# Optimization experiments

Hardware: AMD Instinct MI355X
Metric: run time of the kernel (lower is better)

## Reference

```python
import jax, jax.numpy as jnp
import numpy as np

B, S, F_IN, D, H, L, E, DFF, OUT = 16, 512, 46, 256, 8, 6, 8, 1024, 3


def _ln(x, s, b, eps=1e-5):
    m = x.mean(-1, keepdims=True)
    v = ((x - m) ** 2).mean(-1, keepdims=True)
    return (x - m) / jnp.sqrt(v + eps) * s + b


def _mha(q_in, kv_in, qkv_w, qkv_b, out_w, out_b, h):
    # torch nn.MultiheadAttention (batch_first), eval mode (no dropout)
    d = q_in.shape[-1]
    dh = d // h
    wq, wk, wv = jnp.split(qkv_w, 3, axis=0)
    bq, bk, bv = jnp.split(qkv_b, 3)
    q = (q_in @ wq.T + bq).reshape(q_in.shape[0], q_in.shape[1], h, dh)
    k = (kv_in @ wk.T + bk).reshape(kv_in.shape[0], kv_in.shape[1], h, dh)
    v = (kv_in @ wv.T + bv).reshape(kv_in.shape[0], kv_in.shape[1], h, dh)
    attn = jax.nn.softmax(jnp.einsum('bqhd,bkhd->bhqk', q, k) / jnp.sqrt(jnp.float32(dh)), axis=-1)
    o = jnp.einsum('bhqk,bkhd->bqhd', attn, v).reshape(q_in.shape[0], q_in.shape[1], d)
    return o @ out_w.T + out_b


def _moe(x, gate_w, gate_b, e_w1, e_b1, e_w2, e_b2, top_k=2):
    # Faithful to source: EVERY expert runs its dense FFN over all tokens,
    # then outputs are mixed by the top-k gate weights (zero for unrouted experts).
    logits = x @ gate_w.T + gate_b                      # (B,S,E)
    tk_logits, tk_idx = jax.lax.top_k(logits, top_k)    # (B,S,K)
    tk_probs = jax.nn.softmax(tk_logits, axis=-1)
    onehot = jax.nn.one_hot(tk_idx, logits.shape[-1], dtype=x.dtype)  # (B,S,K,E)
    weights = (onehot * tk_probs[..., None]).sum(-2)    # (B,S,E)
    hid = jax.nn.gelu(jnp.einsum('bsd,efd->bsef', x, e_w1) + e_b1, approximate=False)  # (B,S,E,DFF)
    out_e = jnp.einsum('bsef,edf->bsed', hid, e_w2) + e_b2                             # (B,S,E,D)
    out = jnp.einsum('bsed,bse->bsd', out_e, weights)
    probs = jax.nn.softmax(logits, axis=-1)
    aux = logits.shape[-1] * jnp.sum(probs.mean(axis=(0, 1)) ** 2)
    return out, aux


def _posenc(s, d):
    pos = jnp.arange(s, dtype=jnp.float32)[:, None]
    div = jnp.exp(jnp.arange(0, d, 2, dtype=jnp.float32) * (-np.log(10000.0) / d))
    pe = jnp.zeros((s, d), jnp.float32)
    pe = pe.at[:, 0::2].set(jnp.sin(pos * div)).at[:, 1::2].set(jnp.cos(pos * div))
    return pe


def _forward(x, in_w, in_b, l_qkv_w, l_qkv_b, l_out_w, l_out_b, gate_w, gate_b,
             e_w1, e_b1, e_w2, e_b2, ln1_s, ln1_b, ln2_s, ln2_b,
             p_qkv_w, p_qkv_b, p_out_w, p_out_b,
             a_w1, a_b1, a_ln1s, a_ln1b, a_w2, a_b2, a_ln2s, a_ln2b, a_w3, a_b3,
             pr_w1, pr_b1, pr_ln1s, pr_ln1b, pr_w2, pr_b2, pr_ln2s, pr_ln2b, pr_w3, pr_b3):
    h = x @ in_w.T + in_b + _posenc(x.shape[1], D)[None]
    aux_total = jnp.float32(0.0)
    # NB: source builds ModuleList([encoder_layer]*L) with the SAME instance -> shared weights
    for _ in range(L):
        attn = _mha(h, h, l_qkv_w, l_qkv_b, l_out_w, l_out_b, H)
        h = _ln(h + attn, ln1_s, ln1_b)
        moe_out, aux = _moe(h, gate_w, gate_b, e_w1, e_b1, e_w2, e_b2)
        aux_total = aux_total + aux
        h = _ln(h + moe_out, ln2_s, ln2_b)
    pooled = _mha(h[:, -1:, :], h, p_qkv_w, p_qkv_b, p_out_w, p_out_b, H)[:, 0]  # (B,D)
    # action head: Linear -> GELU -> LN -> Linear -> GELU -> LN -> Linear
    a = jax.nn.gelu(pooled @ a_w1.T + a_b1, approximate=False)
    a = _ln(a, a_ln1s, a_ln1b)
    a = jax.nn.gelu(a @ a_w2.T + a_b2, approximate=False)
    a = _ln(a, a_ln2s, a_ln2b)
    action = a @ a_w3.T + a_b3
    # profit head: Linear -> LN -> GELU -> Linear -> LN -> GELU -> Linear
    p = jax.nn.gelu(_ln(pooled @ pr_w1.T + pr_b1, pr_ln1s, pr_ln1b), approximate=False)
    p = jax.nn.gelu(_ln(p @ pr_w2.T + pr_b2, pr_ln2s, pr_ln2b), approximate=False)
    profit = p @ pr_w3.T + pr_b3
    return action, profit, aux_total


def setup_inputs() -> dict:
    key = jax.random.key(0)
    ks = iter(jax.random.split(key, 64))
    def w(shape, scale=0.02):
        return jax.random.normal(next(ks), shape, jnp.float32) * scale
    d2, d4 = D // 2, D // 4
    return dict(
        x=jax.random.normal(next(ks), (B, S, F_IN), jnp.float32),
        in_w=w((D, F_IN)), in_b=jnp.zeros(D),
        l_qkv_w=w((3 * D, D)), l_qkv_b=jnp.zeros(3 * D), l_out_w=w((D, D)), l_out_b=jnp.zeros(D),
        gate_w=w((E, D)), gate_b=jnp.zeros(E),
        e_w1=w((E, DFF, D)), e_b1=jnp.zeros((E, DFF)), e_w2=w((E, D, DFF)), e_b2=jnp.zeros((E, D)),
        ln1_s=jnp.ones(D), ln1_b=jnp.zeros(D), ln2_s=jnp.ones(D), ln2_b=jnp.zeros(D),
        p_qkv_w=w((3 * D, D)), p_qkv_b=jnp.zeros(3 * D), p_out_w=w((D, D)), p_out_b=jnp.zeros(D),
        a_w1=w((d2, D)), a_b1=jnp.zeros(d2), a_ln1s=jnp.ones(d2), a_ln1b=jnp.zeros(d2),
        a_w2=w((d4, d2)), a_b2=jnp.zeros(d4), a_ln2s=jnp.ones(d4), a_ln2b=jnp.zeros(d4),
        a_w3=w((OUT, d4)), a_b3=jnp.zeros(OUT),
        pr_w1=w((D, D)), pr_b1=jnp.zeros(D), pr_ln1s=jnp.ones(D), pr_ln1b=jnp.zeros(D),
        pr_w2=w((d2, D)), pr_b2=jnp.zeros(d2), pr_ln2s=jnp.ones(d2), pr_ln2b=jnp.zeros(d2),
        pr_w3=w((1, d2)), pr_b3=jnp.zeros(1),
    )


def reference(x, in_w, in_b, l_qkv_w, l_qkv_b, l_out_w, l_out_b, gate_w, gate_b,
              e_w1, e_b1, e_w2, e_b2, ln1_s, ln1_b, ln2_s, ln2_b,
              p_qkv_w, p_qkv_b, p_out_w, p_out_b,
              a_w1, a_b1, a_ln1s, a_ln1b, a_w2, a_b2, a_ln2s, a_ln2b, a_w3, a_b3,
              pr_w1, pr_b1, pr_ln1s, pr_ln1b, pr_w2, pr_b2, pr_ln2s, pr_ln2b, pr_w3, pr_b3):
    return _forward(x, in_w, in_b, l_qkv_w, l_qkv_b, l_out_w, l_out_b, gate_w, gate_b,
                    e_w1, e_b1, e_w2, e_b2, ln1_s, ln1_b, ln2_s, ln2_b,
                    p_qkv_w, p_qkv_b, p_out_w, p_out_b,
                    a_w1, a_b1, a_ln1s, a_ln1b, a_w2, a_b2, a_ln2s, a_ln2b, a_w3, a_b3,
                    pr_w1, pr_b1, pr_ln1s, pr_ln1b, pr_w2, pr_b2, pr_ln2s, pr_ln2b, pr_w3, pr_b3)
```

## Files before the change

### kernel.cpp

```cpp
#include <hip/hip_runtime.h>
#include <hip/hip_bf16.h>
#include <math.h>


typedef __bf16 bf16;
typedef __bf16 bf16x8 __attribute__((ext_vector_type(8)));
typedef __bf16 bf16x4 __attribute__((ext_vector_type(4)));
typedef float f32x4 __attribute__((ext_vector_type(4)));

#define NIN 41

#define GLOAD_LDS(g, l)                                                    \
    __builtin_amdgcn_global_load_lds(                                      \
        (const __attribute__((address_space(1))) void*)(g),                \
        (__attribute__((address_space(3))) void*)(l), 16, 0, 0)

struct InTab {
    const void* src[NIN];
    unsigned off[NIN];
    unsigned n[NIN];
};

__device__ __forceinline__ float gelu_exact(float x) {
    return 0.5f * x * (1.0f + erff(x * 0.70710678118654752f));
}

__global__ void sniff_kernel(const unsigned* __restrict__ xw, int* __restrict__ flag) {
    __shared__ int cnt;
    if (threadIdx.x == 0) cnt = 0;
    __syncthreads();
    const unsigned w = xw[threadIdx.x];
    const unsigned ex = (w >> 7) & 0xFFu;
    if (ex >= 107u && ex <= 133u) atomicAdd(&cnt, 1);
    __syncthreads();
    if (threadIdx.x == 0) *flag = (cnt >= 192) ? 1 : 0;
}

__global__ __launch_bounds__(256) void convert_kernel(
    InTab tab, bf16* __restrict__ dst_base, const int* __restrict__ flag) {
    const unsigned g0 = blockIdx.x * 1024u;
    int inp = 0;
#pragma unroll
    for (int i = 1; i < NIN; i++)
        if (g0 >= tab.off[i]) inp = i;
    const unsigned n = tab.n[inp];
    const unsigned i0 = g0 - tab.off[inp] + threadIdx.x * 4u;
    if (i0 >= n) return;
    const int isbf = *flag;
    bf16* dst = dst_base + tab.off[inp];
    const unsigned end = (i0 + 4u > n) ? n : i0 + 4u;
    if (isbf) {
        const unsigned short* s = (const unsigned short*)tab.src[inp];
        for (unsigned i = i0; i < end; i++) ((unsigned short*)dst)[i] = s[i];
    } else {
        const float* s = (const float*)tab.src[inp];
        for (unsigned i = i0; i < end; i++) dst[i] = (bf16)s[i];
    }
}

__global__ void out_convert_kernel(const float* __restrict__ st,
                                   const float* __restrict__ auxsums,
                                   void* __restrict__ out,
                                   const int* __restrict__ flag) {
    const int i = threadIdx.x;
    if (i >= 65) return;
    float v;
    if (i == 64) {
        float tot = 0.0f;
        for (int l = 0; l < 6; l++)
            for (int e = 0; e < 8; e++) {
                const float mn = auxsums[l * 8 + e] * (1.0f / 8192.0f);
                tot += 8.0f * mn * mn;
            }
        v = tot;
    } else {
        v = st[i];
    }
    if (*flag) ((bf16*)out)[i] = (bf16)v;
    else       ((float*)out)[i] = v;
}

#define SWZ(r, c) (((r) * 8 + ((c) ^ ((r) & 7))) * 8)

template <int BM, int BN, int WM, int WN, bool VTOUT>
__global__ __launch_bounds__(256) void gemm_bt(
    const bf16* __restrict__ A, const bf16* __restrict__ W,
    const bf16* __restrict__ bias, bf16* __restrict__ C,
    int M, int N, int K, bf16* __restrict__ vT) {
    constexpr int BK = 64;
    __shared__ alignas(16) bf16 As[BM * BK];
    __shared__ alignas(16) bf16 Ws[BN * BK];
    const int bm0 = blockIdx.x * BM, bn0 = blockIdx.y * BN;
    const int tid = threadIdx.x;
    const int wave = tid >> 6, lane = tid & 63;
    constexpr int WCOLS = BN / WN;
    const int wm0 = (wave / WCOLS) * WM, wn0 = (wave % WCOLS) * WN;
    constexpr int MT = WM / 16, NT = WN / 16;
    f32x4 acc[MT][NT] = {};
    const int frow = lane & 15, fquad = lane >> 4;

    constexpr int AIT = BM / 32, BIT = BN / 32;
    const bf16* ag[AIT];
    const bf16* bg[BIT];
    unsigned al[AIT], bl[BIT];
#pragma unroll
    for (int i = 0; i < AIT; i++) {
        const int d = wave * (BM * 2) + i * 64 + lane;
        const int r = d >> 3, c = ((d & 7) ^ (r & 7)) * 8;
        ag[i] = A + (size_t)(bm0 + r) * K + c;
        al[i] = (unsigned)(wave * (BM * 2) + i * 64) * 8u;
    }
#pragma unroll
    for (int i = 0; i < BIT; i++) {
        const int d = wave * (BN * 2) + i * 64 + lane;
        const int r = d >> 3, c = ((d & 7) ^ (r & 7)) * 8;
        bg[i] = W + (size_t)(bn0 + r) * K + c;
        bl[i] = (unsigned)(wave * (BN * 2) + i * 64) * 8u;
    }

    for (int k0 = 0; k0 < K; k0 += BK) {
#pragma unroll
        for (int i = 0; i < AIT; i++) GLOAD_LDS(ag[i] + k0, &As[al[i]]);
#pragma unroll
        for (int i = 0; i < BIT; i++) GLOAD_LDS(bg[i] + k0, &Ws[bl[i]]);
        __syncthreads();
#pragma unroll
        for (int ks = 0; ks < BK / 32; ks++) {
            bf16x8 af[MT], bfr[NT];
#pragma unroll
            for (int mt = 0; mt < MT; mt++) {
                const int r = wm0 + mt * 16 + frow;
                af[mt] = *(const bf16x8*)&As[SWZ(r, ks * 4 + fquad)];
            }
#pragma unroll
            for (int nt = 0; nt < NT; nt++) {
                const int r = wn0 + nt * 16 + frow;
                bfr[nt] = *(const bf16x8*)&Ws[SWZ(r, ks * 4 + fquad)];
            }
#pragma unroll
            for (int mt = 0; mt < MT; mt++)
#pragma unroll
                for (int nt = 0; nt < NT; nt++)
                    acc[mt][nt] = __builtin_amdgcn_mfma_f32_16x16x32_bf16(
                        af[mt], bfr[nt], acc[mt][nt], 0, 0, 0);
        }
        __syncthreads();
    }

#pragma unroll
    for (int mt = 0; mt < MT; mt++)
#pragma unroll
        for (int nt = 0; nt < NT; nt++) {
            const int gn = bn0 + wn0 + nt * 16 + frow;
            const float bv = (float)bias[gn];
#pragma unroll
            for (int r = 0; r < 4; r++) {
                const int gm = bm0 + wm0 + mt * 16 + fquad * 4 + r;
                const float v = acc[mt][nt][r] + bv;
                if (VTOUT && gn >= 512) {
                    const int d = gn - 512;
                    const int bb = gm >> 9, s = gm & 511;
                    vT[((size_t)(bb * 8 + (d >> 5)) * 32 + (d & 31)) * 512 + s] = (bf16)v;
                } else {
                    C[(size_t)gm * N + gn] = (bf16)v;
                }
            }
        }
}

__global__ __launch_bounds__(256) void gemm_moe_w1(
    const bf16* __restrict__ A, const bf16* __restrict__ Wb,
    const bf16* __restrict__ biasb, bf16* __restrict__ hid0,
    bf16* __restrict__ hid1, const int* __restrict__ list,
    const int* __restrict__ tile_ex, const int* __restrict__ ntiles) {
    constexpr int BM = 128, BN = 128, BK = 64, WM = 64, WN = 64;
    constexpr int N = 1024, K = 256;
    const int slot = (blockIdx.x >= 71) ? 1 : 0;
    const int xi = blockIdx.x - slot * 71;
    if (xi >= ntiles[slot]) return;
    __shared__ alignas(16) bf16 As[BM * BK];
    __shared__ alignas(16) bf16 Ws[BN * BK];
    const int* mylist = list + slot * 9216;
    const int e = tile_ex[slot * 72 + xi];
    const bf16* W = Wb + (size_t)e * N * K;
    const bf16* bias = biasb + e * N;
    bf16* C = slot ? hid1 : hid0;
    const int bm0 = xi * BM, bn0 = blockIdx.y * BN;
    const int tid = threadIdx.x;
    const int wave = tid >> 6, lane = tid & 63;
    constexpr int WCOLS = BN / WN;
    const int wm0 = (wave / WCOLS) * WM, wn0 = (wave % WCOLS) * WN;
    constexpr int MT = WM / 16, NT = WN / 16;
    f32x4 acc[MT][NT] = {};
    const int frow = lane & 15, fquad = lane >> 4;

    const bf16* ag[4];
    const bf16* bg[4];
    unsigned al[4], bl[4];
#pragma unroll
    for (int i = 0; i < 4; i++) {
        const int d = wave * 256 + i * 64 + lane;
        const int r = d >> 3, c = ((d & 7) ^ (r & 7)) * 8;
        ag[i] = A + (size_t)mylist[bm0 + r] * K + c;
        al[i] = (unsigned)(wave * 256 + i * 64) * 8u;
        bg[i] = W + (size_t)(bn0 + r) * K + c;
        bl[i] = al[i];
    }

    for (int k0 = 0; k0 < K; k0 += BK) {
#pragma unroll
        for (int i = 0; i < 4; i++) GLOAD_LDS(ag[i] + k0, &As[al[i]]);
#pragma unroll
        for (int i = 0; i < 4; i++) GLOAD_LDS(bg[i] + k0, &Ws[bl[i]]);
        __syncthreads();
#pragma unroll
        for (int ks = 0; ks < 2; ks++) {
            bf16x8 af[MT], bfr[NT];
#pragma unroll
            for (int mt = 0; mt < MT; mt++) {
                const int r = wm0 + mt * 16 + frow;
                af[mt] = *(const bf16x8*)&As[SWZ(r, ks * 4 + fquad)];
            }
#pragma unroll
            for (int nt = 0; nt < NT; nt++) {
                const int r = wn0 + nt * 16 + frow;
                bfr[nt] = *(const bf16x8*)&Ws[SWZ(r, ks * 4 + fquad)];
            }
#pragma unroll
            for (int mt = 0; mt < MT; mt++)
#pragma unroll
                for (int nt = 0; nt < NT; nt++)
                    acc[mt][nt] = __builtin_amdgcn_mfma_f32_16x16x32_bf16(
                        af[mt], bfr[nt], acc[mt][nt], 0, 0, 0);
        }
        __syncthreads();
    }

#pragma unroll
    for (int mt = 0; mt < MT; mt++)
#pragma unroll
        for (int nt = 0; nt < NT; nt++) {
            const int gn = bn0 + wn0 + nt * 16 + frow;
            const float bv = (float)bias[gn];
#pragma unroll
            for (int r = 0; r < 4; r++) {
                const int gm = bm0 + wm0 + mt * 16 + fquad * 4 + r;
                C[(size_t)gm * N + gn] = (bf16)gelu_exact(acc[mt][nt][r] + bv);
            }
        }
}

__global__ __launch_bounds__(256) void gemm_moe_w2(
    const bf16* __restrict__ hid0, const bf16* __restrict__ hid1,
    const bf16* __restrict__ Wb, const bf16* __restrict__ biasb,
    bf16* __restrict__ moe0, bf16* __restrict__ moe1,
    const int* __restrict__ list, const float* __restrict__ lw,
    const int* __restrict__ tile_ex, const int* __restrict__ ntiles) {
    constexpr int BM = 128, BN = 64, BK = 64, WM = 32;
    constexpr int N = 256, K = 1024;
    const int slot = (blockIdx.x >= 71) ? 1 : 0;
    const int xi = blockIdx.x - slot * 71;
    if (xi >= ntiles[slot]) return;
    __shared__ alignas(16) bf16 As[BM * BK];
    __shared__ alignas(16) bf16 Ws[BN * BK];
    const bf16* A = slot ? hid1 : hid0;
    bf16* C = slot ? moe1 : moe0;
    const int* mylist = list + slot * 9216;
    const float* mylw = lw + slot * 9216;
    const int e = tile_ex[slot * 72 + xi];
    const bf16* W = Wb + (size_t)e * N * K;
    const bf16* bias = biasb + e * N;
    const int bm0 = xi * BM, bn0 = blockIdx.y * BN;
    const int tid = threadIdx.x;
    const int wave = tid >> 6, lane = tid & 63;
    const int wm0 = wave * WM;
    constexpr int MT = WM / 16, NT = 4;
    f32x4 acc[MT][NT] = {};
    const int frow = lane & 15, fquad = lane >> 4;

    const bf16* ag[4];
    const bf16* bg[2];
    unsigned al[4], bl[2];
#pragma unroll
    for (int i = 0; i < 4; i++) {
        const int d = wave * 256 + i * 64 + lane;
        const int r = d >> 3, c = ((d & 7) ^ (r & 7)) * 8;
        ag[i] = A + (size_t)(bm0 + r) * K + c;
        al[i] = (unsigned)(wave * 256 + i * 64) * 8u;
    }
#pragma unroll
    for (int i = 0; i < 2; i++) {
        const int d = wave * 128 + i * 64 + lane;
        const int r = d >> 3, c = ((d & 7) ^ (r & 7)) * 8;
        bg[i] = W + (size_t)(bn0 + r) * K + c;
        bl[i] = (unsigned)(wave * 128 + i * 64) * 8u;
    }

    for (int k0 = 0; k0 < K; k0 += BK) {
#pragma unroll
        for (int i = 0; i < 4; i++) GLOAD_LDS(ag[i] + k0, &As[al[i]]);
#pragma unroll
        for (int i = 0; i < 2; i++) GLOAD_LDS(bg[i] + k0, &Ws[bl[i]]);
        __syncthreads();
#pragma unroll
        for (int ks = 0; ks < 2; ks++) {
            bf16x8 af[MT], bfr[NT];
#pragma unroll
            for (int mt = 0; mt < MT; mt++) {
                const int r = wm0 + mt * 16 + frow;
                af[mt] = *(const bf16x8*)&As[SWZ(r, ks * 4 + fquad)];
            }
#pragma unroll
            for (int nt = 0; nt < NT; nt++) {
                const int r = nt * 16 + frow;
                bfr[nt] = *(const bf16x8*)&Ws[SWZ(r, ks * 4 + fquad)];
            }
#pragma unroll
            for (int mt = 0; mt < MT; mt++)
#pragma unroll
                for (int nt = 0; nt < NT; nt++)
                    acc[mt][nt] = __builtin_amdgcn_mfma_f32_16x16x32_bf16(
                        af[mt], bfr[nt], acc[mt][nt], 0, 0, 0);
        }
        __syncthreads();
    }

#pragma unroll
    for (int mt = 0; mt < MT; mt++)
#pragma unroll
        for (int nt = 0; nt < NT; nt++) {
            const int gn = bn0 + nt * 16 + frow;
            const float bv = (float)bias[gn];
#pragma unroll
            for (int r = 0; r < 4; r++) {
                const int gm = bm0 + wm0 + mt * 16 + fquad * 4 + r;
                const float v = acc[mt][nt][r] + bv;
                C[(size_t)mylist[gm] * 256 + gn] = (bf16)(mylw[gm] * v);
            }
        }
}

__global__ __launch_bounds__(256) void input_proj_kernel(
    const bf16* __restrict__ x, const bf16* __restrict__ w,
    const bf16* __restrict__ b, bf16* __restrict__ h) {
    const int m = blockIdx.x, t = threadIdx.x;
    __shared__ float xs[46];
    if (t < 46) xs[t] = (float)x[m * 46 + t];
    __syncthreads();
    float acc = (float)b[t];
#pragma unroll
    for (int k = 0; k < 46; k++) acc += xs[k] * (float)w[t * 46 + k];
    const int s = m & 511;
    const int i = t >> 1;
    const float dv = expf((float)(2 * i) * (-9.210340371976184f / 256.0f));
    const float ang = (float)s * dv;
    const float pe = (t & 1) ? cosf(ang) : sinf(ang);
    h[(size_t)m * 256 + t] = (bf16)(acc + pe);
}

__global__ __launch_bounds__(256) void ln_kernel(
    bf16* __restrict__ h, const bf16* __restrict__ a0,
    const bf16* __restrict__ a1, const bf16* __restrict__ s,
    const bf16* __restrict__ b) {
    const int wv = threadIdx.x >> 6, lane = threadIdx.x & 63;
    const int m = blockIdx.x * 8 + wv * 2 + (lane >> 5);
    const int c0 = (lane & 31) * 8;
    const size_t off = (size_t)m * 256 + c0;
    bf16x8 hv = *(const bf16x8*)&h[off];
    bf16x8 av = *(const bf16x8*)&a0[off];
    bf16x8 bv2 = *(const bf16x8*)&a1[off];
    float x[8];
    float s1 = 0.0f, s2 = 0.0f;
#pragma unroll
    for (int j = 0; j < 8; j++) {
        x[j] = (float)hv[j] + (float)av[j] + (float)bv2[j];
        s1 += x[j];
        s2 += x[j] * x[j];
    }
#pragma unroll
    for (int msk = 1; msk < 32; msk <<= 1) {
        s1 += __shfl_xor(s1, msk, 64);
        s2 += __shfl_xor(s2, msk, 64);
    }
    const float mean = s1 * (1.0f / 256.0f);
    const float var = fmaxf(s2 * (1.0f / 256.0f) - mean * mean, 0.0f);
    const float inv = rsqrtf(var + 1e-5f);
    bf16x8 sv = *(const bf16x8*)&s[c0];
    bf16x8 bv = *(const bf16x8*)&b[c0];
    bf16x8 o;
#pragma unroll
    for (int j = 0; j < 8; j++)
        o[j] = (bf16)((x[j] - mean) * inv * (float)sv[j] + (float)bv[j]);
    *(bf16x8*)&h[off] = o;
}

__global__ __launch_bounds__(256) void proj_gate_ln_kernel(
    const bf16* __restrict__ A, const bf16* __restrict__ W,
    const bf16* __restrict__ bias, bf16* __restrict__ h,
    const bf16* __restrict__ lns, const bf16* __restrict__ lnb,
    const bf16* __restrict__ gw, const bf16* __restrict__ gb,
    int* __restrict__ top_e, float* __restrict__ top_w,
    int* __restrict__ g_hist, float* __restrict__ aux_sums) {
    __shared__ alignas(16) bf16 As[32 * 64];
    __shared__ alignas(16) bf16 Ws[256 * 64];
    __shared__ alignas(16) bf16 hs[32 * 264];
    __shared__ alignas(16) bf16 gws[8 * 264];
    __shared__ float rws1[4][32], rws2[4][32];
    __shared__ float meanv[32], invv[32];
    __shared__ float lg[256];
    __shared__ int sh_hist[16];
    __shared__ float sh_aux[8];

    const int bm0 = blockIdx.x * 32;
    const int tid = threadIdx.x;
    const int wave = tid >> 6, lane = tid & 63;
    const int wn0 = (wave & 3) * 64;
    const int frow = lane & 15, fquad = lane >> 4;
    f32x4 acc[2][4] = {};

    const int da = wave * 64 + lane;
    const int ra = da >> 3, ca = ((da & 7) ^ (ra & 7)) * 8;
    const bf16* ag = A + (size_t)(bm0 + ra) * 256 + ca;
    const unsigned al = (unsigned)(wave * 64) * 8u;
    const bf16* bg[8];
    unsigned bl[8];
#pragma unroll
    for (int i = 0; i < 8; i++) {
        const int d = wave * 512 + i * 64 + lane;
        const int r = d >> 3, c = ((d & 7) ^ (r & 7)) * 8;
        bg[i] = W + (size_t)r * 256 + c;
        bl[i] = (unsigned)(wave * 512 + i * 64) * 8u;
    }

    {
        const int rr = tid >> 3, ccb = (tid & 7) * 32;
        const bf16* src = &h[(size_t)(bm0 + rr) * 256 + ccb];
        bf16x8 v0 = *(const bf16x8*)&src[0];
        bf16x8 v1 = *(const bf16x8*)&src[8];
        bf16x8 v2 = *(const bf16x8*)&src[16];
        bf16x8 v3 = *(const bf16x8*)&src[24];
        bf16* dst = &hs[rr * 264 + ccb];
        *(bf16x8*)&dst[0] = v0;
        *(bf16x8*)&dst[8] = v1;
        *(bf16x8*)&dst[16] = v2;
        *(bf16x8*)&dst[24] = v3;
    }
    {
        const int e = tid >> 5, k = (tid & 31) * 8;
        *(bf16x8*)&gws[e * 264 + k] = *(const bf16x8*)&gw[e * 256 + k];
    }
    if (tid < 16) sh_hist[tid] = 0;
    if (tid < 8) sh_aux[tid] = 0.0f;

    for (int k0 = 0; k0 < 256; k0 += 64) {
        GLOAD_LDS(ag + k0, &As[al]);
#pragma unroll
        for (int i = 0; i < 8; i++) GLOAD_LDS(bg[i] + k0, &Ws[bl[i]]);
        __syncthreads();
#pragma unroll
        for (int ks = 0; ks < 2; ks++) {
            bf16x8 af[2], bfr[4];
#pragma unroll
            for (int mt = 0; mt < 2; mt++)
                af[mt] = *(const bf16x8*)&As[SWZ(mt * 16 + frow, ks * 4 + fquad)];
#pragma unroll
            for (int nt = 0; nt < 4; nt++)
                bfr[nt] = *(const bf16x8*)&Ws[SWZ(wn0 + nt * 16 + frow, ks * 4 + fquad)];
#pragma unroll
            for (int mt = 0; mt < 2; mt++)
#pragma unroll
                for (int nt = 0; nt < 4; nt++)
                    acc[mt][nt] = __builtin_amdgcn_mfma_f32_16x16x32_bf16(
                        af[mt], bfr[nt], acc[mt][nt], 0, 0, 0);
        }
        __syncthreads();
    }

    float s1v[2][4] = {}, s2v[2][4] = {};
#pragma unroll
    for (int mt = 0; mt < 2; mt++)
#pragma unroll
        for (int nt = 0; nt < 4; nt++) {
            const int gn = wn0 + nt * 16 + frow;
            const float bv = (float)bias[gn];
#pragma unroll
            for (int r = 0; r < 4; r++) {
                const int row = mt * 16 + fquad * 4 + r;
                const float x = acc[mt][nt][r] + bv + (float)hs[row * 264 + gn];
                acc[mt][nt][r] = x;
                s1v[mt][r] += x;
                s2v[mt][r] += x * x;
            }
        }
#pragma unroll
    for (int mt = 0; mt < 2; mt++)
#pragma unroll
        for (int r = 0; r < 4; r++) {
#pragma unroll
            for (int m = 1; m < 16; m <<= 1) {
                s1v[mt][r] += __shfl_xor(s1v[mt][r], m, 64);
                s2v[mt][r] += __shfl_xor(s2v[mt][r], m, 64);
            }
        }
    if (frow == 0) {
#pragma unroll
        for (int mt = 0; mt < 2; mt++)
#pragma unroll
            for (int r = 0; r < 4; r++) {
                const int row = mt * 16 + fquad * 4 + r;
                rws1[wave][row] = s1v[mt][r];
                rws2[wave][row] = s2v[mt][r];
            }
    }
    __syncthreads();
    if (tid < 32) {
        const float a = rws1[0][tid] + rws1[1][tid] + rws1[2][tid] + rws1[3][tid];
        const float c2 = rws2[0][tid] + rws2[1][tid] + rws2[2][tid] + rws2[3][tid];
        const float mean = a * (1.0f / 256.0f);
        const float var = fmaxf(c2 * (1.0f / 256.0f) - mean * mean, 0.0f);
        meanv[tid] = mean;
        invv[tid] = rsqrtf(var + 1e-5f);
    }
    __syncthreads();

#pragma unroll
    for (int mt = 0; mt < 2; mt++)
#pragma unroll
        for (int nt = 0; nt < 4; nt++) {
            const int gn = wn0 + nt * 16 + frow;
            const float sg = (float)lns[gn], bgn = (float)lnb[gn];
#pragma unroll
            for (int r = 0; r < 4; r++) {
                const int row = mt * 16 + fquad * 4 + r;
                const float o = (acc[mt][nt][r] - meanv[row]) * invv[row] * sg + bgn;
                hs[row * 264 + gn] = (bf16)o;
            }
        }
    __syncthreads();

    {
        const int rr = tid >> 3, ccb = (tid & 7) * 32;
        bf16* dst = &h[(size_t)(bm0 + rr) * 256 + ccb];
        const bf16* src = &hs[rr * 264 + ccb];
        *(bf16x8*)&dst[0] = *(const bf16x8*)&src[0];
        *(bf16x8*)&dst[8] = *(const bf16x8*)&src[8];
        *(bf16x8*)&dst[16] = *(const bf16x8*)&src[16];
        *(bf16x8*)&dst[24] = *(const bf16x8*)&src[24];
    }
    {
        const int row = tid >> 3, e = tid & 7;
        float acg = (float)gb[e];
        for (int k = 0; k < 256; k += 8) {
            bf16x8 hv = *(const bf16x8*)&hs[row * 264 + k];
            bf16x8 wv = *(const bf16x8*)&gws[e * 264 + k];
#pragma unroll
            for (int q = 0; q < 8; q++) acg += (float)hv[q] * (float)wv[q];
        }
        lg[row * 8 + e] = acg;
    }
    __syncthreads();

    if (tid < 32) {
        const int tok = bm0 + tid;
        float l[8];
#pragma unroll
        for (int j = 0; j < 8; j++) l[j] = lg[tid * 8 + j];
        int i0 = 0;
#pragma unroll
        for (int j = 1; j < 8; j++)
            if (l[j] > l[i0]) i0 = j;
        int i1 = -1;
#pragma unroll
        for (int j = 0; j < 8; j++)
            if (j != i0 && (i1 < 0 || l[j] > l[i1])) i1 = j;
        const float p0 = 1.0f / (1.0f + expf(l[i1] - l[i0]));
        top_e[tok] = i0;         top_w[tok] = p0;
        top_e[8192 + tok] = i1;  top_w[8192 + tok] = 1.0f - p0;
        atomicAdd(&sh_hist[i0], 1);
        atomicAdd(&sh_hist[8 + i1], 1);
        const float mx = l[i0];
        float se = 0.0f;
#pragma unroll
        for (int j = 0; j < 8; j++) { l[j] = expf(l[j] - mx); se += l[j]; }
        const float si = 1.0f / se;
#pragma unroll
        for (int j = 0; j < 8; j++) atomicAdd(&sh_aux[j], l[j] * si);
    }
    __syncthreads();
    if (tid < 16) g_hist[blockIdx.x * 16 + tid] = sh_hist[tid];
    if (tid < 8) atomicAdd(&aux_sums[tid], sh_aux[tid]);
}

__global__ __launch_bounds__(256) void scatter_route_kernel(
    const int* __restrict__ g_hist, const int* __restrict__ top_e,
    const float* __restrict__ top_w, int* __restrict__ ntiles,
    int* __restrict__ tile_ex, int* __restrict__ list, float* __restrict__ lw) {
    __shared__ int gh[256][16];
    __shared__ int ps[16][8];
    __shared__ int s_cnt[16], s_pre[16], s_off[16], pos[16];
    const int tid = threadIdx.x;
    for (int i = tid; i < 4096; i += 256) gh[i >> 4][i & 15] = g_hist[i];
    __syncthreads();
    if (tid < 128) {
        const int se = tid >> 3, ch = tid & 7;
        int s = 0;
        for (int b = ch * 32; b < ch * 32 + 32; b++) s += gh[b][se];
        ps[se][ch] = s;
    }
    __syncthreads();
    if (tid < 16) {
        int run = 0;
        for (int ch = 0; ch < 8; ch++) run += ps[tid][ch];
        const int b0 = (int)blockIdx.x * 4;
        int pre = 0;
        for (int ch = 0; ch < (b0 >> 5); ch++) pre += ps[tid][ch];
        for (int b = b0 & ~31; b < b0; b++) pre += gh[b][tid];
        s_cnt[tid] = run;
        s_pre[tid] = pre;
    }
    __syncthreads();
    if (tid < 2) {
        const int slot = tid;
        int o = 0;
        for (int e2 = 0; e2 < 8; e2++) {
            s_off[slot * 8 + e2] = o;
            const int nt = (s_cnt[slot * 8 + e2] + 127) >> 7;
            if (blockIdx.x == 0)
                for (int t = 0; t < nt; t++) tile_ex[slot * 72 + (o >> 7) + t] = e2;
            o += nt << 7;
        }
        if (blockIdx.x == 0) ntiles[slot] = o >> 7;
    }
    __syncthreads();
    if (tid < 16) pos[tid] = s_off[tid] + s_pre[tid];
    __syncthreads();
    if (blockIdx.x == 0) {
        for (int idx = tid; idx < 16 * 128; idx += 256) {
            const int seg = idx >> 7, i = idx & 127;
            const int slot = seg >> 3;
            const int start = s_off[seg] + s_cnt[seg];
            const int end = s_off[seg] + ((s_cnt[seg] + 127) & ~127);
            const int p = start + i;
            if (p < end) {
                list[slot * 9216 + p] = 8192;
                lw[slot * 9216 + p] = 0.0f;
            }
        }
    }
    if (tid < 128) {
        const int tok = blockIdx.x * 128 + tid;
#pragma unroll
        for (int slot = 0; slot < 2; slot++) {
            const int e = top_e[slot * 8192 + tok];
            const float w = top_w[slot * 8192 + tok];
            const int idx = atomicAdd(&pos[slot * 8 + e], 1);
            list[slot * 9216 + idx] = tok;
            lw[slot * 9216 + idx] = w;
        }
    }
}

__global__ __launch_bounds__(256) void attn_kernel(
    const bf16* __restrict__ qkv, const bf16* __restrict__ vT,
    bf16* __restrict__ aout) {
    __shared__ alignas(16) bf16 P[32][520];
    __shared__ float wsum[4][32];
    __shared__ float sinv[32];
    const int s0 = blockIdx.x * 32;
    const int b = blockIdx.y >> 3, hh = blockIdx.y & 7;
    const int tid = threadIdx.x, wave = tid >> 6, lane = tid & 63;
    const int frow = lane & 15, fquad = lane >> 4;
    const size_t base = (size_t)b * 512;
    const float CST = 0.25505654f;

    bf16x8 qf[2];
#pragma unroll
    for (int mt = 0; mt < 2; mt++)
        qf[mt] = *(const bf16x8*)&qkv[(base + s0 + mt * 16 + frow) * 768 + hh * 32 + fquad * 8];
    float rsum[2][4] = {};
#pragma unroll
    for (int k8 = 0; k8 < 8; k8++) {
        const int key0 = (wave * 8 + k8) * 16;
        bf16x8 kf = *(const bf16x8*)&qkv[(base + key0 + frow) * 768 + 256 + hh * 32 + fquad * 8];
#pragma unroll
        for (int mt = 0; mt < 2; mt++) {
            f32x4 c = {};
            c = __builtin_amdgcn_mfma_f32_16x16x32_bf16(qf[mt], kf, c, 0, 0, 0);
#pragma unroll
            for (int r = 0; r < 4; r++) {
                const float e_ = __builtin_exp2f(fminf(c[r] * CST, 60.0f));
                P[mt * 16 + fquad * 4 + r][key0 + frow] = (bf16)e_;
                rsum[mt][r] += e_;
            }
        }
    }
#pragma unroll
    for (int mt = 0; mt < 2; mt++)
#pragma unroll
        for (int r = 0; r < 4; r++) {
#pragma unroll
            for (int m = 1; m < 16; m <<= 1)
                rsum[mt][r] += __shfl_xor(rsum[mt][r], m, 64);
        }
    if (frow == 0) {
#pragma unroll
        for (int mt = 0; mt < 2; mt++)
#pragma unroll
            for (int r = 0; r < 4; r++)
                wsum[wave][mt * 16 + fquad * 4 + r] = rsum[mt][r];
    }
    __syncthreads();
    if (tid < 32)
        sinv[tid] = 1.0f / (wsum[0][tid] + wsum[1][tid] + wsum[2][tid] + wsum[3][tid]);

    {
        const int mt = wave >> 1, nt = wave & 1;
        const bf16* vrow = &vT[((size_t)(b * 8 + hh) * 32 + nt * 16 + frow) * 512];
        f32x4 o = {};
#pragma unroll
        for (int ks = 0; ks < 16; ks++) {
            bf16x8 pf = *(const bf16x8*)&P[mt * 16 + frow][ks * 32 + fquad * 8];
            bf16x8 vf = *(const bf16x8*)&vrow[ks * 32 + fquad * 8];
            o = __builtin_amdgcn_mfma_f32_16x16x32_bf16(pf, vf, o, 0, 0, 0);
        }
        __syncthreads();
        const int r0 = mt * 16 + fquad * 4;
#pragma unroll
        for (int r = 0; r < 4; r++)
            aout[(base + s0 + r0 + r) * 256 + hh * 32 + nt * 16 + frow] =
                (bf16)(o[r] * sinv[r0 + r]);
    }
}

__global__ __launch_bounds__(256) void pooled_attn_kernel(
    const bf16* __restrict__ qkv, const bf16* __restrict__ vT,
    float* __restrict__ pattn) {
    __shared__ float p_lds[512];
    __shared__ float wmax[4], wsum[4];
    const int b = blockIdx.x >> 3, hh = blockIdx.x & 7;
    const int tid = threadIdx.x, wave = tid >> 6, lane = tid & 63;
    const size_t base = (size_t)b * 512;
    const float scale = 0.17677669529663687f;

    bf16x8 qv[4];
#pragma unroll
    for (int i = 0; i < 4; i++)
        qv[i] = *(const bf16x8*)&qkv[(base + 511) * 768 + hh * 32 + i * 8];

    float s[2];
    float mx = -1e30f;
#pragma unroll
    for (int j = 0; j < 2; j++) {
        const int key = wave * 128 + j * 64 + lane;
        const bf16* kr = &qkv[(base + key) * 768 + 256 + hh * 32];
        float acc = 0.0f;
#pragma unroll
        for (int i = 0; i < 4; i++) {
            bf16x8 kv = *(const bf16x8*)&kr[i * 8];
#pragma unroll
            for (int q = 0; q < 8; q++) acc += (float)qv[i][q] * (float)kv[q];
        }
        s[j] = acc * scale;
        mx = fmaxf(mx, s[j]);
    }
#pragma unroll
    for (int m = 1; m < 64; m <<= 1) mx = fmaxf(mx, __shfl_xor(mx, m, 64));
    if (lane == 0) wmax[wave] = mx;
    __syncthreads();
    const float bmx = fmaxf(fmaxf(wmax[0], wmax[1]), fmaxf(wmax[2], wmax[3]));
    float se = 0.0f;
#pragma unroll
    for (int j = 0; j < 2; j++) {
        s[j] = expf(s[j] - bmx);
        se += s[j];
        p_lds[wave * 128 + j * 64 + lane] = s[j];
    }
#pragma unroll
    for (int m = 1; m < 64; m <<= 1) se += __shfl_xor(se, m, 64);
    if (lane == 0) wsum[wave] = se;
    __syncthreads();
    const float inv = 1.0f / (wsum[0] + wsum[1] + wsum[2] + wsum[3]);

    const int d = tid >> 3, seg = tid & 7;
    const bf16* vr = &vT[((size_t)(b * 8 + hh) * 32 + d) * 512 + seg * 64];
    const float* pp = &p_lds[seg * 64];
    float o = 0.0f;
#pragma unroll
    for (int i = 0; i < 64; i += 8) {
        bf16x8 vv = *(const bf16x8*)&vr[i];
#pragma unroll
        for (int q = 0; q < 8; q++) o += pp[i + q] * (float)vv[q];
    }
#pragma unroll
    for (int m = 1; m < 8; m <<= 1) o += __shfl_xor(o, m, 64);
    if (seg == 0) pattn[b * 256 + hh * 32 + d] = o * inv;
}

__global__ __launch_bounds__(256) void heads_kernel(
    const float* __restrict__ pattn,
    const bf16* __restrict__ pout_w, const bf16* __restrict__ pout_b,
    const bf16* __restrict__ aw1, const bf16* __restrict__ ab1,
    const bf16* __restrict__ aln1s, const bf16* __restrict__ aln1b,
    const bf16* __restrict__ aw2, const bf16* __restrict__ ab2,
    const bf16* __restrict__ aln2s, const bf16* __restrict__ aln2b,
    const bf16* __restrict__ aw3, const bf16* __restrict__ ab3,
    const bf16* __restrict__ pw1, const bf16* __restrict__ pb1,
    const bf16* __restrict__ pln1s, const bf16* __restrict__ pln1b,
    const bf16* __restrict__ pw2, const bf16* __restrict__ pb2,
    const bf16* __restrict__ pln2s, const bf16* __restrict__ pln2b,
    const bf16* __restrict__ pw3, const bf16* __restrict__ pb3,
    float* __restrict__ out) {
    const int b = blockIdx.x, t = threadIdx.x;
    __shared__ float pa_s[256];
    __shared__ float pool[256], buf[256], buf2[256], r1[256], r2[256];
    pa_s[t] = pattn[b * 256 + t];
    __syncthreads();

    {
        float a = (float)pout_b[t];
        const bf16* wr = &pout_w[t * 256];
        for (int k = 0; k < 256; k += 8) {
            bf16x8 wv = *(const bf16x8*)&wr[k];
#pragma unroll
            for (int q = 0; q < 8; q++) a += pa_s[k + q] * (float)wv[q];
        }
        pool[t] = a;
    }
    __syncthreads();

    auto block_ln = [&](float* v, int W, const bf16* ls, const bf16* lb) {
        const float val = (t < W) ? v[t] : 0.0f;
        r1[t] = val;
        r2[t] = val * val;
        __syncthreads();
        for (int off = 128; off > 0; off >>= 1) {
            if (t < off) { r1[t] += r1[t + off]; r2[t] += r2[t + off]; }
            __syncthreads();
        }
        const float mean = r1[0] / (float)W;
        const float var = fmaxf(r2[0] / (float)W - mean * mean, 0.0f);
        const float inv = rsqrtf(var + 1e-5f);
        __syncthreads();
        if (t < W) v[t] = (val - mean) * inv * (float)ls[t] + (float)lb[t];
        __syncthreads();
    };

    if (t < 128) {
        float a = (float)ab1[t];
        const bf16* wr = &aw1[t * 256];
        for (int k = 0; k < 256; k += 8) {
            bf16x8 wv = *(const bf16x8*)&wr[k];
#pragma unroll
            for (int q = 0; q < 8; q++) a += pool[k + q] * (float)wv[q];
        }
        buf[t] = gelu_exact(a);
    }
    __syncthreads();
    block_ln(buf, 128, aln1s, aln1b);
    if (t < 64) {
        float a = (float)ab2[t];
        const bf16* wr = &aw2[t * 128];
        for (int k = 0; k < 128; k += 8) {
            bf16x8 wv = *(const bf16x8*)&wr[k];
#pragma unroll
            for (int q = 0; q < 8; q++) a += buf[k + q] * (float)wv[q];
        }
        buf2[t] = gelu_exact(a);
    }
    __syncthreads();
    block_ln(buf2, 64, aln2s, aln2b);
    if (t < 3) {
        float a = (float)ab3[t];
        for (int k = 0; k < 64; k++) a += buf2[k] * (float)aw3[t * 64 + k];
        out[b * 3 + t] = a;
    }

    {
        float a = (float)pb1[t];
        const bf16* wr = &pw1[t * 256];
        for (int k = 0; k < 256; k += 8) {
            bf16x8 wv = *(const bf16x8*)&wr[k];
#pragma unroll
            for (int q = 0; q < 8; q++) a += pool[k + q] * (float)wv[q];
        }
        buf[t] = a;
    }
    __syncthreads();
    block_ln(buf, 256, pln1s, pln1b);
    buf[t] = gelu_exact(buf[t]);
    __syncthreads();
    if (t < 128) {
        float a = (float)pb2[t];
        const bf16* wr = &pw2[t * 256];
        for (int k = 0; k < 256; k += 8) {
            bf16x8 wv = *(const bf16x8*)&wr[k];
#pragma unroll
            for (int q = 0; q < 8; q++) a += buf[k + q] * (float)wv[q];
        }
        buf2[t] = a;
    }
    __syncthreads();
    block_ln(buf2, 128, pln2s, pln2b);
    if (t < 128) buf2[t] = gelu_exact(buf2[t]);
    __syncthreads();
    if (t == 0) {
        float a = (float)pb3[0];
        for (int k = 0; k < 128; k++) a += buf2[k] * (float)pw3[k];
        out[48 + b] = a;
    }
}

extern "C" void kernel_launch(void* const* d_in, const int* in_sizes, int n_in,
                              void* d_out, int out_size, void* d_ws, size_t ws_size,
                              hipStream_t stream) {
    char* ws = (char*)d_ws;
    const size_t MB = 1024 * 1024;
    bf16*  h     = (bf16*)(ws);
    bf16*  moe0  = (bf16*)(ws + 8 * MB);
    bf16*  moe1  = (bf16*)(ws + 13 * MB);
    char*  ctrl  = ws + 20 * MB;
    float* auxs   = (float*)(ctrl + 0);
    int*   flag   = (int*)(ctrl + 192);
    int*   ntiles = (int*)(ctrl + 256);
    int*   tileex = (int*)(ctrl + 320);
    float* ostage = (float*)(ctrl + 1024);
    int*   g_hist = (int*)(ctrl + 2048);
    int*   top_e  = (int*)(ctrl + 20480);
    float* top_w  = (float*)(ctrl + 86016);
    int*   list   = (int*)(ctrl + 151552);
    float* lw     = (float*)(ctrl + 225280);
    bf16*  qkv   = (bf16*)(ws + 24 * MB);
    bf16*  aoutb = (bf16*)(ws + 40 * MB);
    bf16*  hid0  = (bf16*)(ws + 56 * MB);
    bf16*  hid1  = (bf16*)(ws + 80 * MB);
    bf16*  vT    = (bf16*)(ws + 104 * MB);
    float* pattn = (float*)(ws + 110 * MB);
    bf16*  cvbase = (bf16*)(ws + 112 * MB);

    InTab tab;
    unsigned off = 0;
    bf16* cv[NIN];
    for (int i = 0; i < NIN; i++) {
        tab.src[i] = d_in[i];
        tab.off[i] = off;
        tab.n[i] = (unsigned)in_sizes[i];
        cv[i] = cvbase + off;
        off += ((unsigned)in_sizes[i] + 1023u) & ~1023u;
    }
    const int cv_blocks = (int)(off >> 10);

    const bf16 *x = cv[0], *in_w = cv[1], *in_b = cv[2], *qkv_w = cv[3], *qkv_b = cv[4],
               *out_w = cv[5], *out_b = cv[6], *gate_w = cv[7], *gate_b = cv[8],
               *e_w1 = cv[9], *e_b1 = cv[10], *e_w2 = cv[11], *e_b2 = cv[12],
               *ln1_s = cv[13], *ln1_b = cv[14], *ln2_s = cv[15], *ln2_b = cv[16],
               *pqkv_w = cv[17], *pqkv_b = cv[18], *pout_w = cv[19], *pout_b = cv[20],
               *a_w1 = cv[21], *a_b1 = cv[22], *a_ln1s = cv[23], *a_ln1b = cv[24],
               *a_w2 = cv[25], *a_b2 = cv[26], *a_ln2s = cv[27], *a_ln2b = cv[28],
               *a_w3 = cv[29], *a_b3 = cv[30],
               *pr_w1 = cv[31], *pr_b1 = cv[32], *pr_ln1s = cv[33], *pr_ln1b = cv[34],
               *pr_w2 = cv[35], *pr_b2 = cv[36], *pr_ln2s = cv[37], *pr_ln2b = cv[38],
               *pr_w3 = cv[39], *pr_b3 = cv[40];

    sniff_kernel<<<1, 256, 0, stream>>>((const unsigned*)d_in[0], flag);
    convert_kernel<<<cv_blocks, 256, 0, stream>>>(tab, cvbase, flag);

    hipMemsetAsync(auxs, 0, 192, stream);
    input_proj_kernel<<<8192, 256, 0, stream>>>(x, in_w, in_b, h);

    for (int l = 0; l < 6; l++) {
        gemm_bt<64, 128, 32, 64, true><<<dim3(128, 6), 256, 0, stream>>>(
            h, qkv_w, qkv_b, qkv, 8192, 768, 256, vT);
        attn_kernel<<<dim3(16, 128), 256, 0, stream>>>(qkv, vT, aoutb);
        proj_gate_ln_kernel<<<256, 256, 0, stream>>>(
            aoutb, out_w, out_b, h, ln1_s, ln1_b, gate_w, gate_b,
            top_e, top_w, g_hist, auxs + l * 8);
        scatter_route_kernel<<<64, 256, 0, stream>>>(g_hist, top_e, top_w,
                                                     ntiles, tileex, list, lw);
        gemm_moe_w1<<<dim3(142, 8), 256, 0, stream>>>(
            h, e_w1, e_b1, hid0, hid1, list, tileex, ntiles);
        gemm_moe_w2<<<dim3(142, 4), 256, 0, stream>>>(
            hid0, hid1, e_w2, e_b2, moe0, moe1, list, lw, tileex, ntiles);
        ln_kernel<<<1024, 256, 0, stream>>>(h, moe0, moe1, ln2_s, ln2_b);
    }

    gemm_bt<64, 128, 32, 64, true><<<dim3(128, 6), 256, 0, stream>>>(
        h, pqkv_w, pqkv_b, qkv, 8192, 768, 256, vT);
    pooled_attn_kernel<<<128, 256, 0, stream>>>(qkv, vT, pattn);
    heads_kernel<<<16, 256, 0, stream>>>(
        pattn, pout_w, pout_b,
        a_w1, a_b1, a_ln1s, a_ln1b, a_w2, a_b2, a_ln2s, a_ln2b, a_w3, a_b3,
        pr_w1, pr_b1, pr_ln1s, pr_ln1b, pr_w2, pr_b2, pr_ln2s, pr_ln2b, pr_w3, pr_b3,
        ostage);
    out_convert_kernel<<<1, 128, 0, stream>>>(ostage, auxs, d_out, flag);
}
```

Baseline: 997.3 us.

## Double-buffer LDS tiles in GEMM kernels to overlap loads with MFMA

Gives the four GEMM-style kernels (the generic bt GEMM, both MoE expert GEMMs and the projection+gate+LN kernel) two LDS buffers for the A and W tiles. The next K-tile is issued with global_load_lds into the other buffer before the MFMAs on the current tile, and the per-iteration pre-compute barrier is removed. The goal is to hide global-load latency behind matrix work. In exchange LDS use per block doubles, which can lower the number of resident blocks per CU. The end-of-loop barrier still waits on the prefetch, so overlap is limited to within one iteration.

```diff
diff --git a/kernel.cpp b/kernel.cpp
--- a/kernel.cpp
+++ b/kernel.cpp
@@ -88,8 +88,8 @@
     const bf16* __restrict__ bias, bf16* __restrict__ C,
     int M, int N, int K, bf16* __restrict__ vT) {
     constexpr int BK = 64;
-    __shared__ alignas(16) bf16 As[BM * BK];
-    __shared__ alignas(16) bf16 Ws[BN * BK];
+    __shared__ alignas(16) bf16 As[2][BM * BK];
+    __shared__ alignas(16) bf16 Ws[2][BN * BK];
     const int bm0 = blockIdx.x * BM, bn0 = blockIdx.y * BN;
     const int tid = threadIdx.x;
     const int wave = tid >> 6, lane = tid & 63;
@@ -118,24 +118,30 @@
         bl[i] = (unsigned)(wave * (BN * 2) + i * 64) * 8u;
     }
 
+    auto stage = [&](int buf, int k0) {
+#pragma unroll
+        for (int i = 0; i < AIT; i++) GLOAD_LDS(ag[i] + k0, &As[buf][al[i]]);
+#pragma unroll
+        for (int i = 0; i < BIT; i++) GLOAD_LDS(bg[i] + k0, &Ws[buf][bl[i]]);
+    };
+
+    stage(0, 0);
+    __syncthreads();
+    int cur = 0;
     for (int k0 = 0; k0 < K; k0 += BK) {
-#pragma unroll
-        for (int i = 0; i < AIT; i++) GLOAD_LDS(ag[i] + k0, &As[al[i]]);
-#pragma unroll
-        for (int i = 0; i < BIT; i++) GLOAD_LDS(bg[i] + k0, &Ws[bl[i]]);
-        __syncthreads();
+        if (k0 + BK < K) stage(cur ^ 1, k0 + BK);
 #pragma unroll
         for (int ks = 0; ks < BK / 32; ks++) {
             bf16x8 af[MT], bfr[NT];
 #pragma unroll
             for (int mt = 0; mt < MT; mt++) {
                 const int r = wm0 + mt * 16 + frow;
-                af[mt] = *(const bf16x8*)&As[SWZ(r, ks * 4 + fquad)];
+                af[mt] = *(const bf16x8*)&As[cur][SWZ(r, ks * 4 + fquad)];
             }
 #pragma unroll
             for (int nt = 0; nt < NT; nt++) {
                 const int r = wn0 + nt * 16 + frow;
-                bfr[nt] = *(const bf16x8*)&Ws[SWZ(r, ks * 4 + fquad)];
+                bfr[nt] = *(const bf16x8*)&Ws[cur][SWZ(r, ks * 4 + fquad)];
             }
 #pragma unroll
             for (int mt = 0; mt < MT; mt++)
@@ -145,6 +151,7 @@
                         af[mt], bfr[nt], acc[mt][nt], 0, 0, 0);
         }
         __syncthreads();
+        cur ^= 1;
     }
 
 #pragma unroll
@@ -178,8 +185,8 @@
     const int slot = (blockIdx.x >= 71) ? 1 : 0;
     const int xi = blockIdx.x - slot * 71;
     if (xi >= ntiles[slot]) return;
-    __shared__ alignas(16) bf16 As[BM * BK];
-    __shared__ alignas(16) bf16 Ws[BN * BK];
+    __shared__ alignas(16) bf16 As[2][BM * BK];
+    __shared__ alignas(16) bf16 Ws[2][BN * BK];
     const int* mylist = list + slot * 9216;
     const int e = tile_ex[slot * 72 + xi];
     const bf16* W = Wb + (size_t)e * N * K;
@@ -207,24 +214,30 @@
         bl[i] = al[i];
     }
 
+    auto stage = [&](int buf, int k0) {
+#pragma unroll
+        for (int i = 0; i < 4; i++) GLOAD_LDS(ag[i] + k0, &As[buf][al[i]]);
+#pragma unroll
+        for (int i = 0; i < 4; i++) GLOAD_LDS(bg[i] + k0, &Ws[buf][bl[i]]);
+    };
+
+    stage(0, 0);
+    __syncthreads();
+    int cur = 0;
     for (int k0 = 0; k0 < K; k0 += BK) {
-#pragma unroll
-        for (int i = 0; i < 4; i++) GLOAD_LDS(ag[i] + k0, &As[al[i]]);
-#pragma unroll
-        for (int i = 0; i < 4; i++) GLOAD_LDS(bg[i] + k0, &Ws[bl[i]]);
-        __syncthreads();
+        if (k0 + BK < K) stage(cur ^ 1, k0 + BK);
 #pragma unroll
         for (int ks = 0; ks < 2; ks++) {
             bf16x8 af[MT], bfr[NT];
 #pragma unroll
             for (int mt = 0; mt < MT; mt++) {
                 const int r = wm0 + mt * 16 + frow;
-                af[mt] = *(const bf16x8*)&As[SWZ(r, ks * 4 + fquad)];
+                af[mt] = *(const bf16x8*)&As[cur][SWZ(r, ks * 4 + fquad)];
             }
 #pragma unroll
             for (int nt = 0; nt < NT; nt++) {
                 const int r = wn0 + nt * 16 + frow;
-                bfr[nt] = *(const bf16x8*)&Ws[SWZ(r, ks * 4 + fquad)];
+                bfr[nt] = *(const bf16x8*)&Ws[cur][SWZ(r, ks * 4 + fquad)];
             }
 #pragma unroll
             for (int mt = 0; mt < MT; mt++)
@@ -234,6 +247,7 @@
                         af[mt], bfr[nt], acc[mt][nt], 0, 0, 0);
         }
         __syncthreads();
+        cur ^= 1;
     }
 
 #pragma unroll
@@ -261,8 +275,8 @@
     const int slot = (blockIdx.x >= 71) ? 1 : 0;
     const int xi = blockIdx.x - slot * 71;
     if (xi >= ntiles[slot]) return;
-    __shared__ alignas(16) bf16 As[BM * BK];
-    __shared__ alignas(16) bf16 Ws[BN * BK];
+    __shared__ alignas(16) bf16 As[2][BM * BK];
+    __shared__ alignas(16) bf16 Ws[2][BN * BK];
     const bf16* A = slot ? hid1 : hid0;
     bf16* C = slot ? moe1 : moe0;
     const int* mylist = list + slot * 9216;
@@ -296,24 +310,30 @@
         bl[i] = (unsigned)(wave * 128 + i * 64) * 8u;
     }
 
+    auto stage = [&](int buf, int k0) {
+#pragma unroll
+        for (int i = 0; i < 4; i++) GLOAD_LDS(ag[i] + k0, &As[buf][al[i]]);
+#pragma unroll
+        for (int i = 0; i < 2; i++) GLOAD_LDS(bg[i] + k0, &Ws[buf][bl[i]]);
+    };
+
+    stage(0, 0);
+    __syncthreads();
+    int cur = 0;
     for (int k0 = 0; k0 < K; k0 += BK) {
-#pragma unroll
-        for (int i = 0; i < 4; i++) GLOAD_LDS(ag[i] + k0, &As[al[i]]);
-#pragma unroll
-        for (int i = 0; i < 2; i++) GLOAD_LDS(bg[i] + k0, &Ws[bl[i]]);
-        __syncthreads();
+        if (k0 + BK < K) stage(cur ^ 1, k0 + BK);
 #pragma unroll
         for (int ks = 0; ks < 2; ks++) {
             bf16x8 af[MT], bfr[NT];
 #pragma unroll
             for (int mt = 0; mt < MT; mt++) {
                 const int r = wm0 + mt * 16 + frow;
-                af[mt] = *(const bf16x8*)&As[SWZ(r, ks * 4 + fquad)];
+                af[mt] = *(const bf16x8*)&As[cur][SWZ(r, ks * 4 + fquad)];
             }
 #pragma unroll
             for (int nt = 0; nt < NT; nt++) {
                 const int r = nt * 16 + frow;
-                bfr[nt] = *(const bf16x8*)&Ws[SWZ(r, ks * 4 + fquad)];
+                bfr[nt] = *(const bf16x8*)&Ws[cur][SWZ(r, ks * 4 + fquad)];
             }
 #pragma unroll
             for (int mt = 0; mt < MT; mt++)
@@ -323,6 +343,7 @@
                         af[mt], bfr[nt], acc[mt][nt], 0, 0, 0);
         }
         __syncthreads();
+        cur ^= 1;
     }
 
 #pragma unroll
@@ -401,8 +422,8 @@
     const bf16* __restrict__ gw, const bf16* __restrict__ gb,
     int* __restrict__ top_e, float* __restrict__ top_w,
     int* __restrict__ g_hist, float* __restrict__ aux_sums) {
-    __shared__ alignas(16) bf16 As[32 * 64];
-    __shared__ alignas(16) bf16 Ws[256 * 64];
+    __shared__ alignas(16) bf16 As[2][32 * 64];
+    __shared__ alignas(16) bf16 Ws[2][256 * 64];
     __shared__ alignas(16) bf16 hs[32 * 264];
     __shared__ alignas(16) bf16 gws[8 * 264];
     __shared__ float rws1[4][32], rws2[4][32];
@@ -431,6 +452,14 @@
         bg[i] = W + (size_t)r * 256 + c;
         bl[i] = (unsigned)(wave * 512 + i * 64) * 8u;
     }
+
+    auto stage = [&](int buf, int k0) {
+        GLOAD_LDS(ag + k0, &As[buf][al]);
+#pragma unroll
+        for (int i = 0; i < 8; i++) GLOAD_LDS(bg[i] + k0, &Ws[buf][bl[i]]);
+    };
+
+    stage(0, 0);
 
     {
         const int rr = tid >> 3, ccb = (tid & 7) * 32;
@@ -451,21 +480,20 @@
     }
     if (tid < 16) sh_hist[tid] = 0;
     if (tid < 8) sh_aux[tid] = 0.0f;
-
+    __syncthreads();
+
+    int cur = 0;
     for (int k0 = 0; k0 < 256; k0 += 64) {
-        GLOAD_LDS(ag + k0, &As[al]);
-#pragma unroll
-        for (int i = 0; i < 8; i++) GLOAD_LDS(bg[i] + k0, &Ws[bl[i]]);
-        __syncthreads();
+        if (k0 + 64 < 256) stage(cur ^ 1, k0 + 64);
 #pragma unroll
         for (int ks = 0; ks < 2; ks++) {
             bf16x8 af[2], bfr[4];
 #pragma unroll
             for (int mt = 0; mt < 2; mt++)
-                af[mt] = *(const bf16x8*)&As[SWZ(mt * 16 + frow, ks * 4 + fquad)];
+                af[mt] = *(const bf16x8*)&As[cur][SWZ(mt * 16 + frow, ks * 4 + fquad)];
 #pragma unroll
             for (int nt = 0; nt < 4; nt++)
-                bfr[nt] = *(const bf16x8*)&Ws[SWZ(wn0 + nt * 16 + frow, ks * 4 + fquad)];
+                bfr[nt] = *(const bf16x8*)&Ws[cur][SWZ(wn0 + nt * 16 + frow, ks * 4 + fquad)];
 #pragma unroll
             for (int mt = 0; mt < 2; mt++)
 #pragma unroll
@@ -474,6 +502,7 @@
                         af[mt], bfr[nt], acc[mt][nt], 0, 0, 0);
         }
         __syncthreads();
+        cur ^= 1;
     }
 
     float s1v[2][4] = {}, s2v[2][4] = {};
```

Measured after the change: 1.054 ms. 1.06x slower.

## Stage GEMM epilogues through LDS for vectorized stores and use polynomial GELU

Applied to the files above, without the earlier changes.

The GEMM epilogues now write the bias-added results into shared memory, which reuses the operand tile buffers, and then emit coalesced 16-byte row stores instead of scattered 2-byte stores. The V-transpose path writes 4-element vectors along the sequence axis. The MoE first layer swaps erff for an Abramowitz-Stegun polynomial GELU built on exp2, and the second layer hoists its per-row gate weights into registers. The changes add a barrier and an LDS round trip per tile. The polynomial GELU is an approximation with error around 1e-7, which is below bf16 precision.

```diff
diff --git a/kernel.cpp b/kernel.cpp
--- a/kernel.cpp
+++ b/kernel.cpp
@@ -23,6 +23,16 @@
 
 __device__ __forceinline__ float gelu_exact(float x) {
     return 0.5f * x * (1.0f + erff(x * 0.70710678118654752f));
+}
+
+__device__ __forceinline__ float gelu_fast(float x) {
+    const float u = fabsf(x) * 0.70710678118654752f;
+    const float t = 1.0f / (1.0f + 0.3275911f * u);
+    const float p = t * (0.254829592f + t * (-0.284496736f + t * (1.421413741f +
+                    t * (-1.453152027f + t * 1.061405429f))));
+    const float er = 1.0f - p * __builtin_exp2f(-u * u * 1.4426950408889634f);
+    const float s = (x >= 0.0f) ? er : -er;
+    return 0.5f * x * (1.0f + s);
 }
 
 __global__ void sniff_kernel(const unsigned* __restrict__ xw, int* __restrict__ flag) {
@@ -88,8 +98,9 @@
     const bf16* __restrict__ bias, bf16* __restrict__ C,
     int M, int N, int K, bf16* __restrict__ vT) {
     constexpr int BK = 64;
-    __shared__ alignas(16) bf16 As[BM * BK];
-    __shared__ alignas(16) bf16 Ws[BN * BK];
+    __shared__ alignas(16) bf16 smem[BM * BK + BN * BK];
+    bf16* As = smem;
+    bf16* Ws = smem + BM * BK;
     const int bm0 = blockIdx.x * BM, bn0 = blockIdx.y * BN;
     const int tid = threadIdx.x;
     const int wave = tid >> 6, lane = tid & 63;
@@ -147,25 +158,46 @@
         __syncthreads();
     }
 
-#pragma unroll
-    for (int mt = 0; mt < MT; mt++)
-#pragma unroll
-        for (int nt = 0; nt < NT; nt++) {
-            const int gn = bn0 + wn0 + nt * 16 + frow;
-            const float bv = (float)bias[gn];
-#pragma unroll
-            for (int r = 0; r < 4; r++) {
-                const int gm = bm0 + wm0 + mt * 16 + fquad * 4 + r;
-                const float v = acc[mt][nt][r] + bv;
-                if (VTOUT && gn >= 512) {
-                    const int d = gn - 512;
-                    const int bb = gm >> 9, s = gm & 511;
-                    vT[((size_t)(bb * 8 + (d >> 5)) * 32 + (d & 31)) * 512 + s] = (bf16)v;
-                } else {
-                    C[(size_t)gm * N + gn] = (bf16)v;
-                }
-            }
-        }
+    if (VTOUT && bn0 >= 512) {
+#pragma unroll
+        for (int mt = 0; mt < MT; mt++)
+#pragma unroll
+            for (int nt = 0; nt < NT; nt++) {
+                const int gn = bn0 + wn0 + nt * 16 + frow;
+                const float bv = (float)bias[gn];
+                bf16x4 o4;
+#pragma unroll
+                for (int r = 0; r < 4; r++) o4[r] = (bf16)(acc[mt][nt][r] + bv);
+                const int gm0 = bm0 + wm0 + mt * 16 + fquad * 4;
+                const int d = gn - 512;
+                *(bf16x4*)&vT[((size_t)((gm0 >> 9) * 8 + (d >> 5)) * 32 + (d & 31)) * 512 +
+                              (gm0 & 511)] = o4;
+            }
+    } else {
+        bf16* Cs = smem;
+#pragma unroll
+        for (int mt = 0; mt < MT; mt++)
+#pragma unroll
+            for (int nt = 0; nt < NT; nt++) {
+                const int cl = wn0 + nt * 16 + frow;
+                const float bv = (float)bias[bn0 + cl];
+#pragma unroll
+                for (int r = 0; r < 4; r++)
+                    Cs[(wm0 + mt * 16 + fquad * 4 + r) * BN + cl] =
+                        (bf16)(acc[mt][nt][r] + bv);
+            }
+        __syncthreads();
+        constexpr int CPR = BN / 8;
+        constexpr int CH = (BM * BN) / (256 * 8);
+#pragma unroll
+        for (int i = 0; i < CH; i++) {
+            const int ch = tid + i * 256;
+            const int row = ch / CPR;
+            const int col = (ch % CPR) * 8;
+            *(bf16x8*)&C[(size_t)(bm0 + row) * N + bn0 + col] =
+                *(const bf16x8*)&Cs[row * BN + col];
+        }
+    }
 }
 
 __global__ __launch_bounds__(256) void gemm_moe_w1(
@@ -178,8 +210,9 @@
     const int slot = (blockIdx.x >= 71) ? 1 : 0;
     const int xi = blockIdx.x - slot * 71;
     if (xi >= ntiles[slot]) return;
-    __shared__ alignas(16) bf16 As[BM * BK];
-    __shared__ alignas(16) bf16 Ws[BN * BK];
+    __shared__ alignas(16) bf16 smem[BM * BK + BN * BK];
+    bf16* As = smem;
+    bf16* Ws = smem + BM * BK;
     const int* mylist = list + slot * 9216;
     const int e = tile_ex[slot * 72 + xi];
     const bf16* W = Wb + (size_t)e * N * K;
@@ -236,18 +269,29 @@
         __syncthreads();
     }
 
-#pragma unroll
-    for (int mt = 0; mt < MT; mt++)
-#pragma unroll
-        for (int nt = 0; nt < NT; nt++) {
-            const int gn = bn0 + wn0 + nt * 16 + frow;
-            const float bv = (float)bias[gn];
-#pragma unroll
-            for (int r = 0; r < 4; r++) {
-                const int gm = bm0 + wm0 + mt * 16 + fquad * 4 + r;
-                C[(size_t)gm * N + gn] = (bf16)gelu_exact(acc[mt][nt][r] + bv);
-            }
-        }
+    {
+        bf16* Cs = smem;
+#pragma unroll
+        for (int mt = 0; mt < MT; mt++)
+#pragma unroll
+            for (int nt = 0; nt < NT; nt++) {
+                const int cl = wn0 + nt * 16 + frow;
+                const float bv = (float)bias[bn0 + cl];
+#pragma unroll
+                for (int r = 0; r < 4; r++)
+                    Cs[(wm0 + mt * 16 + fquad * 4 + r) * BN + cl] =
+                        (bf16)gelu_fast(acc[mt][nt][r] + bv);
+            }
+        __syncthreads();
+#pragma unroll
+        for (int i = 0; i < 8; i++) {
+            const int ch = tid + i * 256;
+            const int row = ch >> 4;
+            const int col = (ch & 15) * 8;
+            *(bf16x8*)&C[(size_t)(bm0 + row) * N + bn0 + col] =
+                *(const bf16x8*)&Cs[row * BN + col];
+        }
+    }
 }
 
 __global__ __launch_bounds__(256) void gemm_moe_w2(
@@ -261,8 +305,9 @@
     const int slot = (blockIdx.x >= 71) ? 1 : 0;
     const int xi = blockIdx.x - slot * 71;
     if (xi >= ntiles[slot]) return;
-    __shared__ alignas(16) bf16 As[BM * BK];
-    __shared__ alignas(16) bf16 Ws[BN * BK];
+    __shared__ alignas(16) bf16 smem[BM * BK + BN * BK];
+    bf16* As = smem;
+    bf16* Ws = smem + BM * BK;
     const bf16* A = slot ? hid1 : hid0;
     bf16* C = slot ? moe1 : moe0;
     const int* mylist = list + slot * 9216;
@@ -325,19 +370,35 @@
         __syncthreads();
     }
 
-#pragma unroll
-    for (int mt = 0; mt < MT; mt++)
-#pragma unroll
-        for (int nt = 0; nt < NT; nt++) {
-            const int gn = bn0 + nt * 16 + frow;
-            const float bv = (float)bias[gn];
-#pragma unroll
-            for (int r = 0; r < 4; r++) {
-                const int gm = bm0 + wm0 + mt * 16 + fquad * 4 + r;
-                const float v = acc[mt][nt][r] + bv;
-                C[(size_t)mylist[gm] * 256 + gn] = (bf16)(mylw[gm] * v);
-            }
-        }
+    {
+        bf16* Cs = smem;
+        float lwv[MT][4];
+#pragma unroll
+        for (int mt = 0; mt < MT; mt++)
+#pragma unroll
+            for (int r = 0; r < 4; r++)
+                lwv[mt][r] = mylw[bm0 + wm0 + mt * 16 + fquad * 4 + r];
+#pragma unroll
+        for (int mt = 0; mt < MT; mt++)
+#pragma unroll
+            for (int nt = 0; nt < NT; nt++) {
+                const int cl = nt * 16 + frow;
+                const float bv = (float)bias[bn0 + cl];
+#pragma unroll
+                for (int r = 0; r < 4; r++)
+                    Cs[(wm0 + mt * 16 + fquad * 4 + r) * BN + cl] =
+                        (bf16)(lwv[mt][r] * (acc[mt][nt][r] + bv));
+            }
+        __syncthreads();
+#pragma unroll
+        for (int i = 0; i < 4; i++) {
+            const int ch = tid + i * 256;
+            const int row = ch >> 3;
+            const int col = (ch & 7) * 8;
+            *(bf16x8*)&C[(size_t)mylist[bm0 + row] * 256 + bn0 + col] =
+                *(const bf16x8*)&Cs[row * BN + col];
+        }
+    }
 }
 
 __global__ __launch_bounds__(256) void input_proj_kernel(
```

Measured after the change: 1.007 ms. No clear change (+0.9%).
